# Kernel optimization log

Hardware: AMD Instinct MI355X
Metric: run time of the kernel (lower is better)

Reference implementation:

```python
import jax, jax.numpy as jnp
import numpy as np

HID, NH = 2048, 16
QLR, KVLR = 1536, 512
DR, DN, DQK, DV = 64, 128, 192, 128
S = 2048
EPS = 1e-06


def rmsnorm(x, w, eps=EPS):
    return x * jax.lax.rsqrt(jnp.mean(x * x, axis=-1, keepdims=True) + eps) * w


def rope_interleave(x, cos, sin):
    # x: [B,H,S,D]; cos/sin: [B,S,D] (unsqueezed to head dim 1)
    b, h, s, d = x.shape
    # DeepSeek-V3 interleave: (d//2, 2) -> transpose -> flatten
    x = x.reshape(b, h, s, d // 2, 2).swapaxes(3, 4).reshape(b, h, s, d)
    c = cos[:, None, :, :]
    sn = sin[:, None, :, :]
    x1, x2 = x[..., : d // 2], x[..., d // 2:]
    rot = jnp.concatenate([-x2, x1], axis=-1)
    return x * c + rot * sn


def setup_inputs() -> dict:
    key = jax.random.key(0)
    ks = jax.random.split(key, 8)
    hidden_states = jax.random.normal(ks[0], (1, S, HID), dtype=jnp.float32)
    # real RoPE tables for the 64-dim rope part
    inv_freq = 1.0 / (10000.0 ** (np.arange(0, DR, 2, dtype=np.float32) / DR))
    pos = np.arange(S, dtype=np.float32)
    freqs = pos[:, None] * inv_freq[None, :]          # [S, DR/2]
    emb = np.concatenate([freqs, freqs], axis=-1)     # [S, DR]
    cos = jnp.asarray(np.cos(emb), dtype=jnp.float32)[None]
    sin = jnp.asarray(np.sin(emb), dtype=jnp.float32)[None]
    w = 0.02
    wq_a = jax.random.normal(ks[1], (QLR, HID), dtype=jnp.float32) * w
    q_a_ln_w = jnp.ones((QLR,), dtype=jnp.float32)
    wq_b = jax.random.normal(ks[2], (NH * DQK, QLR), dtype=jnp.float32) * w
    wkv_a = jax.random.normal(ks[3], (KVLR + DR, HID), dtype=jnp.float32) * w
    kv_a_ln_w = jnp.ones((KVLR,), dtype=jnp.float32)
    wkv_b = jax.random.normal(ks[4], (NH * (DN + DV), KVLR), dtype=jnp.float32) * w
    wo = jax.random.normal(ks[5], (HID, NH * DV), dtype=jnp.float32) * w
    cu_seqlens = jnp.array([0, S // 2, S], dtype=jnp.int32)  # two packed docs
    return {"hidden_states": hidden_states, "cos": cos, "sin": sin,
            "wq_a": wq_a, "q_a_ln_w": q_a_ln_w, "wq_b": wq_b,
            "wkv_a": wkv_a, "kv_a_ln_w": kv_a_ln_w, "wkv_b": wkv_b,
            "wo": wo, "cu_seqlens": cu_seqlens, "max_seqlen": S // 2}


def reference(hidden_states, cos, sin, wq_a, q_a_ln_w, wq_b, wkv_a, kv_a_ln_w,
              wkv_b, wo, cu_seqlens, max_seqlen):
    B, s, _ = hidden_states.shape
    # LoRA-compressed Q: q_a -> RMSNorm -> q_b
    q = rmsnorm(hidden_states @ wq_a.T, q_a_ln_w) @ wq_b.T       # [B,S,NH*DQK]
    q = q.reshape(B, s, NH, DQK).transpose(0, 2, 1, 3)           # [B,NH,S,DQK]
    q_pass, q_rot = q[..., :DN], q[..., DN:]
    # compressed KV with MQA rope part
    ckv = hidden_states @ wkv_a.T                                 # [B,S,KVLR+DR]
    kv_c, k_rot = ckv[..., :KVLR], ckv[..., KVLR:]
    kv = rmsnorm(kv_c, kv_a_ln_w) @ wkv_b.T                       # [B,S,NH*(DN+DV)]
    kv = kv.reshape(B, s, NH, DN + DV).transpose(0, 2, 1, 3)      # [B,NH,S,DN+DV]
    k_pass, v = kv[..., :DN], kv[..., DN:]
    k_rot = k_rot[:, None, :, :]                                  # [B,1,S,DR]
    q_rot = rope_interleave(q_rot, cos, sin)
    k_rot = rope_interleave(k_rot, cos, sin)
    k_rot = jnp.broadcast_to(k_rot, (B, NH, s, DR))
    qf = jnp.concatenate([q_pass, q_rot], axis=-1)                # [B,NH,S,DQK]
    kf = jnp.concatenate([k_pass, k_rot], axis=-1)                # [B,NH,S,DQK]
    # varlen causal attention: block-diagonal per document + causal
    pos = jnp.arange(s)
    seg = jnp.searchsorted(cu_seqlens[1:], pos, side='right')
    mask = (seg[:, None] == seg[None, :]) & (pos[:, None] >= pos[None, :])
    scale = DQK ** -0.5  # flash default: 1/sqrt(q head dim) (v padded to DQK)
    scores = jnp.einsum('bhqd,bhkd->bhqk', qf, kf) * scale
    scores = jnp.where(mask[None, None], scores, jnp.finfo(scores.dtype).min)
    attn = jax.nn.softmax(scores, axis=-1)
    out = jnp.einsum('bhqk,bhkd->bhqd', attn, v)                  # [B,NH,S,DV]
    out = out.transpose(0, 2, 1, 3).reshape(B, s, NH * DV)
    return out @ wo.T
```

## Files before the change

### kernel.cpp

```cpp
#include <hip/hip_runtime.h>

typedef unsigned short u16;
typedef __attribute__((ext_vector_type(8))) short bf16x8;
typedef __attribute__((ext_vector_type(4))) float f32x4;

#define HID 2048
#define NH 16
#define QLR 1536
#define KVLR 512
#define DR 64
#define DN 128
#define DQK 192
#define DV 128
#define SEQ 2048
#define NKVA 2176
#define SCALE 0.07216878364870323f
#define SCL2 0.1041164359699839f
#define THR2 11.541560327111707f

static __device__ __forceinline__ u16 f2bf(float f) {
  unsigned v = __builtin_bit_cast(unsigned, f);
  v = v + 0x7fffu + ((v >> 16) & 1u);
  return (u16)(v >> 16);
}
static __device__ __forceinline__ float bf2f(u16 u) {
  unsigned v = ((unsigned)u) << 16;
  return __builtin_bit_cast(float, v);
}

#define GLOAD16(gp, lp)                                                        \
  __builtin_amdgcn_global_load_lds(                                            \
      (const __attribute__((address_space(1))) void*)(gp),                     \
      (__attribute__((address_space(3))) void*)(lp), 16, 0, 0)

__global__ void k_convert_all(const float* __restrict__ hs, const float* __restrict__ wq_a,
                              const float* __restrict__ wkv_a, const float* __restrict__ wqb,
                              const float* __restrict__ wkvb, const float* __restrict__ wo,
                              u16* __restrict__ hs_bf, u16* __restrict__ wqkva,
                              u16* __restrict__ wqb_bf, u16* __restrict__ wkvb_bf,
                              u16* __restrict__ wo_bf) {
  const long NQ = 4915200;
  long q = (long)blockIdx.x * blockDim.x + threadIdx.x;
  const long stride = (long)gridDim.x * blockDim.x;
  for (; q < NQ; q += stride) {
    const float* src;
    u16* dst;
    long li;
    bool zero = false;
    if (q < 1048576)        { src = hs;   dst = hs_bf;                      li = q; }
    else if (q < 1835008)   { src = wq_a; dst = wqkva;                      li = q - 1048576; }
    else if (q < 2162688)   { li = q - 1835008; src = wkv_a; dst = wqkva + (size_t)QLR * HID;
                              zero = (li >= 294912); }
    else if (q < 3342336)   { src = wqb;  dst = wqb_bf;                     li = q - 2162688; }
    else if (q < 3866624)   { src = wkvb; dst = wkvb_bf;                    li = q - 3342336; }
    else                    { src = wo;   dst = wo_bf;                      li = q - 3866624; }
    u16 o0 = 0, o1 = 0, o2 = 0, o3 = 0;
    if (!zero) {
      const float4 f = *(const float4*)(src + li * 4);
      o0 = f2bf(f.x); o1 = f2bf(f.y); o2 = f2bf(f.z); o3 = f2bf(f.w);
    }
    u16* d = dst + li * 4;
    d[0] = o0; d[1] = o1; d[2] = o2; d[3] = o3;
  }
}

__global__ void k_rmsnorm2(const float* __restrict__ qkva, const float* __restrict__ qw,
                           const float* __restrict__ kvw, u16* __restrict__ q_ln,
                           u16* __restrict__ kv_ln) {
  const int row = blockIdx.x;
  const int which = blockIdx.y;
  const int t = threadIdx.x;
  const int cols = which ? KVLR : QLR;
  const float inv_cols = which ? (1.0f / KVLR) : (1.0f / QLR);
  const float* x = qkva + (size_t)row * NKVA + (which ? QLR : 0);
  const float* w = which ? kvw : qw;
  u16* Y = (which ? kv_ln : q_ln) + (size_t)row * cols;
  float ss = 0.f;
  for (int i = t * 4; i < cols; i += 1024) {
    float4 v = *(const float4*)(x + i);
    ss += v.x * v.x + v.y * v.y + v.z * v.z + v.w * v.w;
  }
#pragma unroll
  for (int m = 1; m < 64; m <<= 1) ss += __shfl_xor(ss, m, 64);
  __shared__ float red[4];
  if ((t & 63) == 0) red[t >> 6] = ss;
  __syncthreads();
  float tot = red[0] + red[1] + red[2] + red[3];
  float r = rsqrtf(tot * inv_cols + 1e-6f);
  for (int i = t * 4; i < cols; i += 1024) {
    float4 v = *(const float4*)(x + i);
    float4 g = *(const float4*)(w + i);
    u16* y = Y + i;
    y[0] = f2bf(v.x * r * g.x);
    y[1] = f2bf(v.y * r * g.y);
    y[2] = f2bf(v.z * r * g.z);
    y[3] = f2bf(v.w * r * g.w);
  }
}

__global__ __launch_bounds__(256) void k_gemm_nt(
    const u16* __restrict__ A, const u16* __restrict__ B, void* __restrict__ Cout,
    int M, int N, int K, int mode) {
  __shared__ __align__(16) u16 As[2][8192];
  __shared__ __align__(16) u16 Bs[2][8192];
  const int t = threadIdx.x;
  const int lane = t & 63;
  const int w = t >> 6, wr = w >> 1, wc = w & 1;
  const int lm = lane & 15, lg = lane >> 4;

  const int nwg = gridDim.x * gridDim.y;
  int bid = blockIdx.y * gridDim.x + blockIdx.x;
  if ((nwg & 7) == 0) bid = (bid & 7) * (nwg >> 3) + (bid >> 3);
  const int bm = bid % gridDim.y;
  const int bn = bid / gridDim.y;

  const int srow = t >> 3;
  const int scol = ((t & 7) ^ (srow & 7)) * 8;
  const u16* aBase = A + (size_t)(bm * 128 + srow) * K + scol;
  const u16* bBase = B + (size_t)(bn * 128 + srow) * K + scol;
  const size_t rowStep = (size_t)32 * K;

#define STAGE(buf, kt_)                                                        \
  do {                                                                         \
    _Pragma("unroll") for (int p = 0; p < 4; ++p) {                            \
      GLOAD16(aBase + (kt_) + p * rowStep, (u16*)As[buf] + p * 2048 + t * 8);  \
      GLOAD16(bBase + (kt_) + p * rowStep, (u16*)Bs[buf] + p * 2048 + t * 8);  \
    }                                                                          \
  } while (0)

  f32x4 acc[4][4] = {};
  const int nk = K >> 6;
  STAGE(0, 0);
  if (nk > 1) STAGE(1, 64);
  int cur = 0;
  for (int kt = 0; kt < nk; ++kt) {
    if (kt + 1 < nk) asm volatile("s_waitcnt vmcnt(8)" ::: "memory");
    else             asm volatile("s_waitcnt vmcnt(0)" ::: "memory");
    __builtin_amdgcn_s_barrier();
    __builtin_amdgcn_sched_barrier(0);
    bf16x8 af[2][4], bfr[2][4];
#pragma unroll
    for (int kk = 0; kk < 2; ++kk) {
#pragma unroll
      for (int i = 0; i < 4; ++i) {
        const int row_ = wr * 64 + i * 16 + lm;
        af[kk][i] = *(const bf16x8*)(As[cur] + row_ * 64 +
                                     ((((kk << 2) | lg) ^ (row_ & 7)) << 3));
      }
#pragma unroll
      for (int j = 0; j < 4; ++j) {
        const int row_ = wc * 64 + j * 16 + lm;
        bfr[kk][j] = *(const bf16x8*)(Bs[cur] + row_ * 64 +
                                      ((((kk << 2) | lg) ^ (row_ & 7)) << 3));
      }
    }
    asm volatile("s_waitcnt lgkmcnt(0)" ::: "memory");
    __builtin_amdgcn_sched_barrier(0);
    __builtin_amdgcn_s_barrier();
    __builtin_amdgcn_sched_barrier(0);
    if (kt + 2 < nk) STAGE(cur, (kt + 2) << 6);
    __builtin_amdgcn_s_setprio(1);
#pragma unroll
    for (int kk = 0; kk < 2; ++kk)
#pragma unroll
      for (int i = 0; i < 4; ++i)
#pragma unroll
        for (int j = 0; j < 4; ++j)
          acc[i][j] = __builtin_amdgcn_mfma_f32_16x16x32_bf16(af[kk][i], bfr[kk][j],
                                                              acc[i][j], 0, 0, 0);
    __builtin_amdgcn_s_setprio(0);
    cur ^= 1;
  }
#undef STAGE

  const int row0 = bm * 128 + wr * 64 + lg * 4;
  const int col0 = bn * 128 + wc * 64 + lm;
  if (mode == 1) {
    u16* C = (u16*)Cout;
#pragma unroll
    for (int i = 0; i < 4; ++i)
#pragma unroll
      for (int r = 0; r < 4; ++r) {
        u16* crow = C + (size_t)(row0 + i * 16 + r) * N + col0;
#pragma unroll
        for (int j = 0; j < 4; ++j) crow[j * 16] = f2bf(acc[i][j][r]);
      }
  } else {
    float* C = (float*)Cout;
#pragma unroll
    for (int i = 0; i < 4; ++i)
#pragma unroll
      for (int r = 0; r < 4; ++r) {
        float* crow = C + (size_t)(row0 + i * 16 + r) * N + col0;
#pragma unroll
        for (int j = 0; j < 4; ++j) crow[j * 16] = acc[i][j][r];
      }
  }
}

template <int WN>
__global__ __launch_bounds__(512) void k_gemm_nt8(
    const u16* __restrict__ A, const u16* __restrict__ B, u16* __restrict__ C,
    int M, int N, int K) {
  constexpr int BN = WN * 64;
  constexpr int NST = 2 + WN;
  __shared__ __align__(16) u16 As[3][128 * 64];
  __shared__ __align__(16) u16 Bs[3][BN * 64];
  const int t = threadIdx.x;
  const int lane = t & 63;
  const int w = t >> 6, wr = w >> 2, wc = w & 3;
  const int lm = lane & 15, lg = lane >> 4;

  const int nwg = gridDim.x * gridDim.y;
  int bid = blockIdx.y * gridDim.x + blockIdx.x;
  if ((nwg & 7) == 0) bid = (bid & 7) * (nwg >> 3) + (bid >> 3);
  const int bm = bid % gridDim.y;
  const int bn = bid / gridDim.y;

  const u16* aT = A + (size_t)bm * 128 * K;
  const u16* bT = B + (size_t)bn * BN * K;

#define STAGE8(buf, kt_)                                                       \
  do {                                                                         \
    _Pragma("unroll") for (int i = 0; i < 2; ++i) {                            \
      const int g = t + i * 512, row = g >> 3, slot = (g & 7) ^ (row & 7);     \
      GLOAD16(aT + (size_t)row * K + slot * 8 + (kt_), (u16*)As[buf] + g * 8); \
    }                                                                          \
    _Pragma("unroll") for (int i = 0; i < WN; ++i) {                           \
      const int g = t + i * 512, row = g >> 3, slot = (g & 7) ^ (row & 7);     \
      GLOAD16(bT + (size_t)row * K + slot * 8 + (kt_), (u16*)Bs[buf] + g * 8); \
    }                                                                          \
  } while (0)

  f32x4 acc[4][WN] = {};
  const int nk = K >> 6;
  STAGE8(0, 0);
  if (nk > 1) STAGE8(1, 64);
  if (nk > 2) STAGE8(2, 128);
  int bt = 0;
  for (int kt = 0; kt < nk; ++kt) {
    const int rem = nk - 1 - kt;
    if (rem >= 2)      asm volatile("s_waitcnt vmcnt(%0)" :: "i"(2 * NST) : "memory");
    else if (rem == 1) asm volatile("s_waitcnt vmcnt(%0)" :: "i"(NST) : "memory");
    else               asm volatile("s_waitcnt vmcnt(0)" ::: "memory");
    __builtin_amdgcn_s_barrier();
    __builtin_amdgcn_sched_barrier(0);
    bf16x8 af[2][4], bfr[2][WN];
#pragma unroll
    for (int kk = 0; kk < 2; ++kk) {
#pragma unroll
      for (int i = 0; i < 4; ++i) {
        const int row_ = wr * 64 + i * 16 + lm;
        af[kk][i] = *(const bf16x8*)(As[bt] + row_ * 64 +
                                     ((((kk << 2) | lg) ^ (row_ & 7)) << 3));
      }
#pragma unroll
      for (int j = 0; j < WN; ++j) {
        const int row_ = wc * (WN * 16) + j * 16 + lm;
        bfr[kk][j] = *(const bf16x8*)(Bs[bt] + row_ * 64 +
                                      ((((kk << 2) | lg) ^ (row_ & 7)) << 3));
      }
    }
    asm volatile("s_waitcnt lgkmcnt(0)" ::: "memory");
    __builtin_amdgcn_sched_barrier(0);
    __builtin_amdgcn_s_barrier();
    __builtin_amdgcn_sched_barrier(0);
    if (kt + 3 < nk) STAGE8(bt, (kt + 3) << 6);
    __builtin_amdgcn_s_setprio(1);
#pragma unroll
    for (int kk = 0; kk < 2; ++kk)
#pragma unroll
      for (int i = 0; i < 4; ++i)
#pragma unroll
        for (int j = 0; j < WN; ++j)
          acc[i][j] = __builtin_amdgcn_mfma_f32_16x16x32_bf16(af[kk][i], bfr[kk][j],
                                                              acc[i][j], 0, 0, 0);
    __builtin_amdgcn_s_setprio(0);
    bt = (bt == 2) ? 0 : bt + 1;
  }
#undef STAGE8

  const int row0 = bm * 128 + wr * 64 + lg * 4;
  const int col0 = bn * BN + wc * (WN * 16) + lm;
#pragma unroll
  for (int i = 0; i < 4; ++i)
#pragma unroll
    for (int r = 0; r < 4; ++r) {
      u16* crow = C + (size_t)(row0 + i * 16 + r) * N + col0;
#pragma unroll
      for (int j = 0; j < WN; ++j) crow[j * 16] = f2bf(acc[i][j][r]);
    }
}

__global__ void k_mk_qf(const u16* __restrict__ qfull, const float* __restrict__ cosb,
                        const float* __restrict__ sinb, u16* __restrict__ qf) {
  const int s = blockIdx.x, h = blockIdx.y, t = threadIdx.x;
  const u16* src = qfull + (size_t)s * (NH * DQK) + h * DQK;
  u16* dst = qf + ((size_t)h * SEQ + s) * DQK;
  dst[t] = f2bf(bf2f(src[t]) * SCL2);
  if (t < 32) {
    float a = bf2f(src[DN + 2 * t]);
    float b = bf2f(src[DN + 2 * t + 1]);
    float c = cosb[(size_t)s * DR + t];
    float sn = sinb[(size_t)s * DR + t];
    dst[DN + t] = f2bf((a * c - b * sn) * SCL2);
    dst[DN + 32 + t] = f2bf((b * c + a * sn) * SCL2);
  }
}

__global__ __launch_bounds__(256) void k_mk_kf_v(
    const u16* __restrict__ kvfull, const float* __restrict__ krot, int krot_stride,
    const float* __restrict__ cosb, const float* __restrict__ sinb,
    u16* __restrict__ kf, u16* __restrict__ vt) {
  __shared__ u16 vts[128][66];
  const int s0 = blockIdx.x * 64, h = blockIdx.y, t = threadIdx.x;
#pragma unroll
  for (int i = 0; i < 8; ++i) {
    const int g = t + i * 256, row = g >> 5, slot = g & 31;
    const u16* src = kvfull + (size_t)(s0 + row) * (NH * 256) + h * 256 + slot * 8;
    bf16x8 v = *(const bf16x8*)src;
    if (slot < 16) {
      *(bf16x8*)(kf + ((size_t)h * SEQ + s0 + row) * DQK + slot * 8) = v;
    } else {
      const int d = (slot - 16) * 8;
#pragma unroll
      for (int e = 0; e < 8; ++e) vts[d + e][row] = (u16)v[e];
    }
  }
#pragma unroll
  for (int i = 0; i < 8; ++i) {
    const int g = t + i * 256, row = g >> 5, c = g & 31;
    float a = krot[(size_t)(s0 + row) * krot_stride + 2 * c];
    float b = krot[(size_t)(s0 + row) * krot_stride + 2 * c + 1];
    float cc = cosb[(size_t)(s0 + row) * DR + c];
    float sn = sinb[(size_t)(s0 + row) * DR + c];
    u16* kd = kf + ((size_t)h * SEQ + s0 + row) * DQK;
    kd[DN + c] = f2bf(a * cc - b * sn);
    kd[DN + 32 + c] = f2bf(b * cc + a * sn);
  }
  __syncthreads();
#pragma unroll
  for (int i = 0; i < 4; ++i) {
    const int g = t + i * 256, d = g >> 3, slot = g & 7;
    bf16x8 v;
#pragma unroll
    for (int e = 0; e < 8; ++e) v[e] = (short)vts[d][slot * 8 + e];
    *(bf16x8*)(vt + ((size_t)h * DV + d) * SEQ + s0 + slot * 8) = v;
  }
}

__global__ __launch_bounds__(256) void k_attn(
    const u16* __restrict__ qf, const u16* __restrict__ kf, const u16* __restrict__ vt,
    u16* __restrict__ attn_out) {
  __shared__ __align__(16) u16 Ks[3][32 * 192];
  __shared__ __align__(16) u16 Vs[3][128 * 32];
  __shared__ __align__(16) u16 p_lds[4][16][32];

  const int t = threadIdx.x, lane = t & 63, w = t >> 6;
  const int lm = lane & 15, lg = lane >> 4;
  const int bid = blockIdx.x;
  const int x = bid & 7, rr = bid >> 3;
  const int i5 = rr & 31, late = rr >> 5;
  const int tj = late ? (i5 >> 2) : 15 - (i5 >> 2);
  const int h = x * 2 + ((i5 >> 1) & 1);
  const int seg = i5 & 1;
  const int tile_row0 = seg * 1024 + tj * 64;
  const int k_begin = seg * 1024;
  const int n_kt = tj * 2 + 2;

  const int lo_row = tile_row0 + w * 16;
  bf16x8 qfr[6];
  {
    const u16* qp = qf + ((size_t)h * SEQ + (lo_row + lm)) * DQK + lg * 8;
#pragma unroll
    for (int c = 0; c < 6; ++c) qfr[c] = *(const bf16x8*)(qp + c * 32);
  }
  int qrow[4];
#pragma unroll
  for (int r = 0; r < 4; ++r) qrow[r] = lo_row + lg * 4 + r;

  float m_r[4], l_loc[4];
#pragma unroll
  for (int r = 0; r < 4; ++r) { m_r[r] = -3.0e4f; l_loc[r] = 0.f; }
  f32x4 oacc[8] = {};
  bf16x8 pa, vv[8];

#define STAGE(buf, kt_)                                                        \
  do {                                                                         \
    const int k0_ = k_begin + (kt_) * 32;                                      \
    _Pragma("unroll") for (int p = 0; p < 3; ++p) {                            \
      const int id = p * 256 + t;                                              \
      const int row = id / 24, colL = id - row * 24;                           \
      const u16* g = kf + ((size_t)h * SEQ + k0_ + row) * DQK +                \
                     ((colL ^ (row & 7)) * 8);                                 \
      GLOAD16(g, (u16*)Ks[buf] + id * 8);                                      \
    }                                                                          \
    _Pragma("unroll") for (int p = 0; p < 2; ++p) {                            \
      const int id = p * 256 + t;                                              \
      const int row = id >> 2, colL = id & 3;                                  \
      const u16* g = vt + ((size_t)h * DV + row) * SEQ + k0_ +                 \
                     ((colL ^ (row & 3)) * 8);                                 \
      GLOAD16(g, (u16*)Vs[buf] + id * 8);                                      \
    }                                                                          \
  } while (0)

#define COMPUTE1(buf, kt_)                                                     \
  do {                                                                         \
    const int k0_ = k_begin + (kt_) * 32;                                      \
    f32x4 sc[2] = {};                                                          \
    __builtin_amdgcn_s_setprio(1);                                             \
    _Pragma("unroll") for (int n0_ = 0; n0_ < 2; ++n0_)                        \
        _Pragma("unroll") for (int c_ = 0; c_ < 6; ++c_) {                     \
      const int row_ = n0_ * 16 + lm, cc_ = c_ * 4 + lg;                       \
      bf16x8 kfr = *(const bf16x8*)(Ks[buf] + row_ * 192 +                     \
                                    ((cc_ ^ (row_ & 7)) * 8));                 \
      sc[n0_] = __builtin_amdgcn_mfma_f32_16x16x32_bf16(qfr[c_], kfr,          \
                                                        sc[n0_], 0, 0, 0);     \
    }                                                                          \
    __builtin_amdgcn_s_setprio(0);                                             \
    float s0a[4], s1a[4];                                                      \
    float over = -1e30f;                                                       \
    if (lo_row >= k0_ + 31) {                                                  \
      _Pragma("unroll") for (int r = 0; r < 4; ++r) {                          \
        s0a[r] = sc[0][r];                                                     \
        s1a[r] = sc[1][r];                                                     \
        over = fmaxf(over, fmaxf(s0a[r], s1a[r]) - m_r[r]);                    \
      }                                                                        \
    } else {                                                                   \
      const int kc0 = k0_ + lm, kc1 = k0_ + 16 + lm;                           \
      _Pragma("unroll") for (int r = 0; r < 4; ++r) {                          \
        s0a[r] = (kc0 <= qrow[r]) ? sc[0][r] : -1e30f;                         \
        s1a[r] = (kc1 <= qrow[r]) ? sc[1][r] : -1e30f;                         \
        over = fmaxf(over, fmaxf(s0a[r], s1a[r]) - m_r[r]);                    \
      }                                                                        \
    }                                                                          \
    if (__any(over > THR2)) {                                                  \
      _Pragma("unroll") for (int r = 0; r < 4; ++r) {                          \
        float mx = fmaxf(s0a[r], s1a[r]);                                      \
        _Pragma("unroll") for (int md = 1; md < 16; md <<= 1)                  \
            mx = fmaxf(mx, __shfl_xor(mx, md, 64));                            \
        float mnew = fmaxf(m_r[r], mx);                                        \
        float alpha = exp2f(m_r[r] - mnew);                                    \
        m_r[r] = mnew;                                                         \
        l_loc[r] *= alpha;                                                     \
        _Pragma("unroll") for (int nd = 0; nd < 8; ++nd) oacc[nd][r] *= alpha; \
      }                                                                        \
    }                                                                          \
    _Pragma("unroll") for (int r = 0; r < 4; ++r) {                            \
      float p0 = exp2f(s0a[r] - m_r[r]);                                       \
      float p1 = exp2f(s1a[r] - m_r[r]);                                       \
      l_loc[r] += p0 + p1;                                                     \
      p_lds[w][lg * 4 + r][lm] = f2bf(p0);                                     \
      p_lds[w][lg * 4 + r][16 + lm] = f2bf(p1);                                \
    }                                                                          \
    asm volatile("s_waitcnt lgkmcnt(0)" ::: "memory");                         \
    __builtin_amdgcn_sched_barrier(0);                                         \
    pa = *(const bf16x8*)(&p_lds[w][lm][lg * 8]);                              \
    _Pragma("unroll") for (int nd = 0; nd < 8; ++nd) {                         \
      const int row_ = nd * 16 + lm;                                           \
      vv[nd] = *(const bf16x8*)(Vs[buf] + row_ * 32 +                          \
                                ((lg ^ (row_ & 3)) * 8));                      \
    }                                                                          \
  } while (0)

  STAGE(0, 0);
  STAGE(1, 1);
  if (n_kt > 2) STAGE(2, 2);
  int bt = 0;
  for (int kt = 0; kt < n_kt; ++kt) {
    const int rem = n_kt - 1 - kt;
    if (rem >= 2)      asm volatile("s_waitcnt vmcnt(10)" ::: "memory");
    else if (rem == 1) asm volatile("s_waitcnt vmcnt(5)" ::: "memory");
    else               asm volatile("s_waitcnt vmcnt(0)" ::: "memory");
    __builtin_amdgcn_s_barrier();
    __builtin_amdgcn_sched_barrier(0);
    COMPUTE1(bt, kt);
    asm volatile("s_waitcnt lgkmcnt(0)" ::: "memory");
    __builtin_amdgcn_sched_barrier(0);
    __builtin_amdgcn_s_barrier();
    __builtin_amdgcn_sched_barrier(0);
    if (kt + 3 < n_kt) STAGE(bt, kt + 3);
    __builtin_amdgcn_s_setprio(1);
#pragma unroll
    for (int nd = 0; nd < 8; ++nd)
      oacc[nd] = __builtin_amdgcn_mfma_f32_16x16x32_bf16(pa, vv[nd], oacc[nd], 0, 0, 0);
    __builtin_amdgcn_s_setprio(0);
    bt = (bt == 2) ? 0 : bt + 1;
  }
#undef STAGE
#undef COMPUTE1

#pragma unroll
  for (int r = 0; r < 4; ++r) {
    float lt = l_loc[r];
#pragma unroll
    for (int md = 1; md < 16; md <<= 1) lt += __shfl_xor(lt, md, 64);
    float inv = 1.0f / lt;
#pragma unroll
    for (int nd = 0; nd < 8; ++nd)
      attn_out[(size_t)qrow[r] * (NH * DV) + h * DV + nd * 16 + lm] =
          f2bf(oacc[nd][r] * inv);
  }
}

extern "C" void kernel_launch(void* const* d_in, const int* in_sizes, int n_in,
                              void* d_out, int out_size, void* d_ws, size_t ws_size,
                              hipStream_t stream) {
  const float* hs = (const float*)d_in[0];
  const float* cosb = (const float*)d_in[1];
  const float* sinb = (const float*)d_in[2];
  const float* wq_a = (const float*)d_in[3];
  const float* q_a_ln_w = (const float*)d_in[4];
  const float* wq_b = (const float*)d_in[5];
  const float* wkv_a = (const float*)d_in[6];
  const float* kv_a_ln_w = (const float*)d_in[7];
  const float* wkv_b = (const float*)d_in[8];
  const float* wo = (const float*)d_in[9];

  char* ws = (char*)d_ws;
  size_t off = 0;
  auto take = [&](size_t bytes) {
    size_t o = off;
    off += (bytes + 255) & ~(size_t)255;
    return o;
  };
  u16* hs_bf = (u16*)(ws + take((size_t)SEQ * HID * 2));
  u16* wqkva = (u16*)(ws + take((size_t)NKVA * HID * 2));
  u16* wqb = (u16*)(ws + take((size_t)(NH * DQK) * QLR * 2));
  u16* wkvb = (u16*)(ws + take((size_t)(NH * 256) * KVLR * 2));
  u16* wo_bf = (u16*)(ws + take((size_t)HID * (NH * DV) * 2));
  float* qkva = (float*)(ws + take((size_t)SEQ * NKVA * 4));
  u16* q_ln = (u16*)(ws + take((size_t)SEQ * QLR * 2));
  u16* kv_ln = (u16*)(ws + take((size_t)SEQ * KVLR * 2));
  u16* qfull = (u16*)(ws + take((size_t)SEQ * NH * DQK * 2));
  u16* kvfull = (u16*)(ws + take((size_t)SEQ * NH * 256 * 2));
  u16* qf = (u16*)(ws + take((size_t)NH * SEQ * DQK * 2));
  u16* kf = (u16*)(ws + take((size_t)NH * SEQ * DQK * 2));
  u16* vt = (u16*)(ws + take((size_t)NH * DV * SEQ * 2));
  u16* attn = (u16*)(ws + take((size_t)SEQ * NH * DV * 2));
  if (off > ws_size) return;

  k_convert_all<<<2048, 256, 0, stream>>>(hs, wq_a, wkv_a, wq_b, wkv_b, wo,
                                          hs_bf, wqkva, wqb, wkvb, wo_bf);

  dim3 g1(NKVA / 128, SEQ / 128);
  k_gemm_nt<<<g1, 256, 0, stream>>>(hs_bf, wqkva, qkva, SEQ, NKVA, HID, 0);

  k_rmsnorm2<<<dim3(SEQ, 2), 256, 0, stream>>>(qkva, q_a_ln_w, kv_a_ln_w, q_ln, kv_ln);

  dim3 g2(NH * DQK / 192, SEQ / 128);
  k_gemm_nt8<3><<<g2, 512, 0, stream>>>(q_ln, wqb, qfull, SEQ, NH * DQK, QLR);
  dim3 g3(NH * 256 / 256, SEQ / 128);
  k_gemm_nt8<4><<<g3, 512, 0, stream>>>(kv_ln, wkvb, kvfull, SEQ, NH * 256, KVLR);

  k_mk_qf<<<dim3(SEQ, NH), 128, 0, stream>>>(qfull, cosb, sinb, qf);
  k_mk_kf_v<<<dim3(SEQ / 64, NH), 256, 0, stream>>>(kvfull, qkva + (QLR + KVLR), NKVA,
                                                    cosb, sinb, kf, vt);

  k_attn<<<512, 256, 0, stream>>>(qf, kf, vt, attn);

  dim3 g4(HID / 128, SEQ / 128);
  k_gemm_nt<<<g4, 256, 0, stream>>>(attn, wo_bf, d_out, SEQ, HID, NH * DV, 0);
}
```

Measured before the change: 187.1 us.

## Fuse Q/K/V prep kernels, use 512-thread GEMM for qkv_a, hoist V reads

Merges the Q scaling and RoPE kernel into the K/V prep kernel so one launch produces qf, kf and vt. The first projection GEMM now uses the 8-wave k_gemm_nt8<2> kernel with a new fp32 output mode. In attention, the V fragment LDS reads move earlier, right after the QK MFMAs, so they overlap with the softmax. The aim is fewer launches, better GEMM throughput and hidden LDS latency, at the cost of more register pressure in attention. The qkv_a GEMM grid uses 17 column tiles of 128, which matches WN=2 (BN=128).

```diff
diff --git a/kernel.cpp b/kernel.cpp
--- a/kernel.cpp
+++ b/kernel.cpp
@@ -200,8 +200,8 @@
 
 template <int WN>
 __global__ __launch_bounds__(512) void k_gemm_nt8(
-    const u16* __restrict__ A, const u16* __restrict__ B, u16* __restrict__ C,
-    int M, int N, int K) {
+    const u16* __restrict__ A, const u16* __restrict__ B, void* __restrict__ Cout,
+    int M, int N, int K, int mode) {
   constexpr int BN = WN * 64;
   constexpr int NST = 2 + WN;
   __shared__ __align__(16) u16 As[3][128 * 64];
@@ -282,36 +282,34 @@
 
   const int row0 = bm * 128 + wr * 64 + lg * 4;
   const int col0 = bn * BN + wc * (WN * 16) + lm;
-#pragma unroll
-  for (int i = 0; i < 4; ++i)
-#pragma unroll
-    for (int r = 0; r < 4; ++r) {
-      u16* crow = C + (size_t)(row0 + i * 16 + r) * N + col0;
-#pragma unroll
-      for (int j = 0; j < WN; ++j) crow[j * 16] = f2bf(acc[i][j][r]);
-    }
-}
-
-__global__ void k_mk_qf(const u16* __restrict__ qfull, const float* __restrict__ cosb,
-                        const float* __restrict__ sinb, u16* __restrict__ qf) {
-  const int s = blockIdx.x, h = blockIdx.y, t = threadIdx.x;
-  const u16* src = qfull + (size_t)s * (NH * DQK) + h * DQK;
-  u16* dst = qf + ((size_t)h * SEQ + s) * DQK;
-  dst[t] = f2bf(bf2f(src[t]) * SCL2);
-  if (t < 32) {
-    float a = bf2f(src[DN + 2 * t]);
-    float b = bf2f(src[DN + 2 * t + 1]);
-    float c = cosb[(size_t)s * DR + t];
-    float sn = sinb[(size_t)s * DR + t];
-    dst[DN + t] = f2bf((a * c - b * sn) * SCL2);
-    dst[DN + 32 + t] = f2bf((b * c + a * sn) * SCL2);
-  }
-}
-
-__global__ __launch_bounds__(256) void k_mk_kf_v(
-    const u16* __restrict__ kvfull, const float* __restrict__ krot, int krot_stride,
+  if (mode == 1) {
+    u16* C = (u16*)Cout;
+#pragma unroll
+    for (int i = 0; i < 4; ++i)
+#pragma unroll
+      for (int r = 0; r < 4; ++r) {
+        u16* crow = C + (size_t)(row0 + i * 16 + r) * N + col0;
+#pragma unroll
+        for (int j = 0; j < WN; ++j) crow[j * 16] = f2bf(acc[i][j][r]);
+      }
+  } else {
+    float* C = (float*)Cout;
+#pragma unroll
+    for (int i = 0; i < 4; ++i)
+#pragma unroll
+      for (int r = 0; r < 4; ++r) {
+        float* crow = C + (size_t)(row0 + i * 16 + r) * N + col0;
+#pragma unroll
+        for (int j = 0; j < WN; ++j) crow[j * 16] = acc[i][j][r];
+      }
+  }
+}
+
+__global__ __launch_bounds__(256) void k_mk_all(
+    const u16* __restrict__ qfull, const u16* __restrict__ kvfull,
+    const float* __restrict__ krot, int krot_stride,
     const float* __restrict__ cosb, const float* __restrict__ sinb,
-    u16* __restrict__ kf, u16* __restrict__ vt) {
+    u16* __restrict__ qf, u16* __restrict__ kf, u16* __restrict__ vt) {
   __shared__ u16 vts[128][66];
   const int s0 = blockIdx.x * 64, h = blockIdx.y, t = threadIdx.x;
 #pragma unroll
@@ -346,6 +344,28 @@
 #pragma unroll
     for (int e = 0; e < 8; ++e) v[e] = (short)vts[d][slot * 8 + e];
     *(bf16x8*)(vt + ((size_t)h * DV + d) * SEQ + s0 + slot * 8) = v;
+  }
+#pragma unroll
+  for (int i = 0; i < 4; ++i) {
+    const int g = t + i * 256, row = g >> 4, vc = g & 15;
+    const u16* src = qfull + (size_t)(s0 + row) * (NH * DQK) + h * DQK + vc * 8;
+    bf16x8 v = *(const bf16x8*)src;
+    bf16x8 o;
+#pragma unroll
+    for (int e = 0; e < 8; ++e) o[e] = (short)f2bf(bf2f((u16)v[e]) * SCL2);
+    *(bf16x8*)(qf + ((size_t)h * SEQ + s0 + row) * DQK + vc * 8) = o;
+  }
+#pragma unroll
+  for (int i = 0; i < 8; ++i) {
+    const int g = t + i * 256, row = g >> 5, c = g & 31;
+    const u16* src = qfull + (size_t)(s0 + row) * (NH * DQK) + h * DQK;
+    float a = bf2f(src[DN + 2 * c]);
+    float b = bf2f(src[DN + 2 * c + 1]);
+    float cc = cosb[(size_t)(s0 + row) * DR + c];
+    float sn = sinb[(size_t)(s0 + row) * DR + c];
+    u16* qd = qf + ((size_t)h * SEQ + s0 + row) * DQK;
+    qd[DN + c] = f2bf((a * cc - b * sn) * SCL2);
+    qd[DN + 32 + c] = f2bf((b * cc + a * sn) * SCL2);
   }
 }
 
@@ -418,6 +438,11 @@
                                                         sc[n0_], 0, 0, 0);     \
     }                                                                          \
     __builtin_amdgcn_s_setprio(0);                                             \
+    _Pragma("unroll") for (int nd = 0; nd < 8; ++nd) {   \
+      const int row_ = nd * 16 + lm;                      \
+      vv[nd] = *(const bf16x8*)(Vs[buf] + row_ * 32 +                          \
+                                ((lg ^ (row_ & 3)) * 8));                      \
+    }                                                                          \
     float s0a[4], s1a[4];                                                      \
     float over = -1e30f;                                                       \
     if (lo_row >= k0_ + 31) {                                                  \
@@ -456,11 +481,6 @@
     asm volatile("s_waitcnt lgkmcnt(0)" ::: "memory");                         \
     __builtin_amdgcn_sched_barrier(0);                                         \
     pa = *(const bf16x8*)(&p_lds[w][lm][lg * 8]);                              \
-    _Pragma("unroll") for (int nd = 0; nd < 8; ++nd) {                         \
-      const int row_ = nd * 16 + lm;                                           \
-      vv[nd] = *(const bf16x8*)(Vs[buf] + row_ * 32 +                          \
-                                ((lg ^ (row_ & 3)) * 8));                      \
-    }                                                                          \
   } while (0)
 
   STAGE(0, 0);
@@ -544,18 +564,17 @@
                                           hs_bf, wqkva, wqb, wkvb, wo_bf);
 
   dim3 g1(NKVA / 128, SEQ / 128);
-  k_gemm_nt<<<g1, 256, 0, stream>>>(hs_bf, wqkva, qkva, SEQ, NKVA, HID, 0);
+  k_gemm_nt8<2><<<g1, 512, 0, stream>>>(hs_bf, wqkva, qkva, SEQ, NKVA, HID, 0);
 
   k_rmsnorm2<<<dim3(SEQ, 2), 256, 0, stream>>>(qkva, q_a_ln_w, kv_a_ln_w, q_ln, kv_ln);
 
   dim3 g2(NH * DQK / 192, SEQ / 128);
-  k_gemm_nt8<3><<<g2, 512, 0, stream>>>(q_ln, wqb, qfull, SEQ, NH * DQK, QLR);
+  k_gemm_nt8<3><<<g2, 512, 0, stream>>>(q_ln, wqb, qfull, SEQ, NH * DQK, QLR, 1);
   dim3 g3(NH * 256 / 256, SEQ / 128);
-  k_gemm_nt8<4><<<g3, 512, 0, stream>>>(kv_ln, wkvb, kvfull, SEQ, NH * 256, KVLR);
-
-  k_mk_qf<<<dim3(SEQ, NH), 128, 0, stream>>>(qfull, cosb, sinb, qf);
-  k_mk_kf_v<<<dim3(SEQ / 64, NH), 256, 0, stream>>>(kvfull, qkva + (QLR + KVLR), NKVA,
-                                                    cosb, sinb, kf, vt);
+  k_gemm_nt8<4><<<g3, 512, 0, stream>>>(kv_ln, wkvb, kvfull, SEQ, NH * 256, KVLR, 1);
+
+  k_mk_all<<<dim3(SEQ / 64, NH), 256, 0, stream>>>(qfull, kvfull, qkva + (QLR + KVLR),
+                                                   NKVA, cosb, sinb, qf, kf, vt);
 
   k_attn<<<512, 256, 0, stream>>>(qf, kf, vt, attn);
 
```

After: 201.6 us. +7.7%, slower.
